# Performance work log

Hardware: AMD Instinct MI355X
Metric: run time of the kernel (lower is better)

## Reference

```python
import jax, jax.numpy as jnp
import numpy as np

STRIDE = 8.0
NUM_CLASSES = 80
IGNORE_THR = 0.5
ANCHORS = np.array([[10.,13.],[16.,30.],[33.,23.]], dtype=np.float32)
TOTAL = np.array([[10.,13.],[16.,30.],[33.,23.],[30.,61.],[62.,45.],[59.,119.],[116.,90.],[156.,198.],[373.,326.]], dtype=np.float32)
# total-anchor index -> local anchor index (anchors_mask = [0,1,2] for this head), else -1
LUT = np.array([0,1,2,-1,-1,-1,-1,-1,-1], dtype=np.int32)


def _safe_log(p):
    # matches torch BCELoss log clamping at -100 (and avoids nan grads at p==0)
    return jnp.where(p > 0, jnp.log(jnp.where(p > 0, p, 1.0)), -100.0)


def _bce(p, t):
    return -(t * _safe_log(p) + (1.0 - t) * _safe_log(1.0 - p))


def _smooth_l1(p, t):
    d = jnp.abs(p - t)
    return jnp.where(d < 1.0, 0.5 * d * d, d - 0.5)


def _iou(b1, b2):
    # center-format (cx, cy, w, h) boxes, broadcastable on leading dims
    b1x1 = b1[..., 0] - b1[..., 2] * 0.5; b1x2 = b1[..., 0] + b1[..., 2] * 0.5
    b1y1 = b1[..., 1] - b1[..., 3] * 0.5; b1y2 = b1[..., 1] + b1[..., 3] * 0.5
    b2x1 = b2[..., 0] - b2[..., 2] * 0.5; b2x2 = b2[..., 0] + b2[..., 2] * 0.5
    b2y1 = b2[..., 1] - b2[..., 3] * 0.5; b2y2 = b2[..., 1] + b2[..., 3] * 0.5
    iw = jnp.clip(jnp.minimum(b1x2, b2x2) - jnp.maximum(b1x1, b2x1), 0.0)
    ih = jnp.clip(jnp.minimum(b1y2, b2y2) - jnp.maximum(b1y1, b2y1), 0.0)
    inter = iw * ih
    a1 = (b1x2 - b1x1) * (b1y2 - b1y1)
    a2 = (b2x2 - b2x1) * (b2y2 - b2y1)
    return inter / (a1 + a2 - inter + 1e-16)


def _forward(input, targets):
    bs, _, in_h, in_w = input.shape
    A, C = ANCHORS.shape[0], NUM_CLASSES
    sa = jnp.asarray(ANCHORS) / STRIDE   # [A,2] scaled anchors
    sta = jnp.asarray(TOTAL) / STRIDE    # [9,2] scaled total anchors
    pred = input.reshape(bs, A, 5 + C, in_h, in_w).transpose(0, 1, 3, 4, 2)  # [B,A,H,W,5+C]
    x = jax.nn.sigmoid(pred[..., 0]); y = jax.nn.sigmoid(pred[..., 1])
    w = pred[..., 2]; h = pred[..., 3]
    conf = jax.nn.sigmoid(pred[..., 4])
    pred_cls = jax.nn.sigmoid(pred[..., 5:])
    gxg = jnp.arange(in_w, dtype=input.dtype)
    gyg = jnp.arange(in_h, dtype=input.dtype)
    pb_x = x + gxg[None, None, None, :]
    pb_y = y + gyg[None, None, :, None]
    pb_w = jnp.exp(w) * sa[None, :, 0, None, None]
    pb_h = jnp.exp(h) * sa[None, :, 1, None, None]
    pred_boxes = jax.lax.stop_gradient(jnp.stack([pb_x, pb_y, pb_w, pb_h], -1))  # [B,A,H,W,4] (.data in torch)

    # ---- get_target, vectorized gather/compute/scatter ----
    T = targets.shape[1]
    valid = jnp.sum(targets, -1) != 0                                     # [B,T]
    gx = targets[..., 1] * in_w; gy = targets[..., 2] * in_h
    gw = targets[..., 3] * in_w; gh = targets[..., 4] * in_h
    gi = gx.astype(jnp.int32); gj = gy.astype(jnp.int32)                  # int() truncation (gx,gy >= 0)
    # anchor matching: IoU of (0,0,gw,gh) against (0,0,aw,ah) for the 9 total anchors
    gt0 = jnp.stack([jnp.zeros_like(gw), jnp.zeros_like(gw), gw, gh], -1)  # [B,T,4]
    an0 = jnp.concatenate([jnp.zeros_like(sta), sta], -1)                  # [9,4]
    a_iou = _iou(gt0[:, :, None, :], an0[None, None, :, :])                # [B,T,9]
    best_n = jnp.argmax(a_iou, -1)                                         # [B,T]
    ai = jnp.asarray(LUT)[best_n]                                          # local anchor index or -1
    write = valid & (ai >= 0)
    ai_w = jnp.where(write, ai, A)                                         # A is OOB -> dropped scatter
    aic = jnp.clip(ai, 0, A - 1)
    # ignore mask: IoU of each gt box against all predicted boxes of its image
    gt = jnp.stack([gx, gy, gw, gh], -1)                                   # [B,T,4]
    p_iou = _iou(gt[:, :, None, None, None, :], pred_boxes[:, None])       # [B,T,A,H,W]
    ignore = jnp.any((p_iou >= IGNORE_THR) & valid[:, :, None, None, None], axis=1)  # [B,A,H,W]
    b_idx = jnp.broadcast_to(jnp.arange(bs)[:, None], (bs, T))
    z = jnp.zeros((bs, A, in_h, in_w), input.dtype)
    def scat(vals):
        return z.at[b_idx, ai_w, gj, gi].set(vals.astype(input.dtype), mode='drop')
    mask = scat(jnp.ones_like(gx))
    scales = scat(2.0 - targets[..., 3] * targets[..., 4])
    tx = scat(gx - gi.astype(input.dtype))
    ty = scat(gy - gj.astype(input.dtype))
    tw = scat(jnp.log(gw / sa[aic, 0] + 1e-16))
    th = scat(jnp.log(gh / sa[aic, 1] + 1e-16))
    cls_idx = targets[..., 0].astype(jnp.int32)
    tcls = jnp.zeros((bs, A, in_h, in_w, C), input.dtype).at[b_idx, ai_w, gj, gi, cls_idx].set(1.0, mode='drop')
    noobj = jnp.minimum(1.0 - ignore.astype(input.dtype), 1.0 - mask)
    n_obj = jnp.sum(valid).astype(input.dtype)

    loss_x = jnp.sum(scales * _bce(x * mask, tx)) / n_obj
    loss_y = jnp.sum(scales * _bce(y * mask, ty)) / n_obj
    loss_w = jnp.sum(scales * _smooth_l1(w * mask, tw)) / n_obj
    loss_h = jnp.sum(scales * _smooth_l1(h * mask, th)) / n_obj
    loss_conf = jnp.sum(_bce(conf * mask, mask)) / n_obj + 0.5 * jnp.sum(_bce(conf * noobj, jnp.zeros_like(conf))) / n_obj
    # bce(pred_cls[mask==1], tcls[mask==1]).sum() == masked full sum (bce>=0, mask binary)
    loss_cls = jnp.sum(mask[..., None] * _bce(pred_cls, tcls)) / n_obj
    loss = 2.5 * (loss_x + loss_y) + 2.5 * (loss_w + loss_h) + 1.0 * loss_conf + 1.0 * loss_cls
    return jnp.stack([loss, loss_x, loss_y, loss_w, loss_h, loss_conf, loss_cls])


def setup_inputs():
    key = jax.random.key(0)
    k1, k2 = jax.random.split(key)
    inp = jax.random.normal(k1, (16, 255, 76, 76), dtype=jnp.float32)
    tgt = jax.random.uniform(k2, (16, 50, 5), dtype=jnp.float32)  # (cls, cx, cy, w, h) in (0,1)
    return {"input": inp, "targets": tgt}


def reference(input, targets):
    return _forward(input, targets)
```

## Files before the change

kernel.cpp:

```cpp
#include <hip/hip_runtime.h>
#include <cstddef>

#define NB 16
#define NT 50
#define NA 3
#define NH 76
#define NW 76
#define NC 80
#define HWSZ (NH*NW)
#define CPB 512
#define NBLKX ((HWSZ + CPB - 1) / CPB)
#define NBLK (NBLKX * NB * NA)
#define NTARG (NB * NT)

__constant__ float d_taw[9] = {1.25f,2.0f,4.125f,3.75f,7.75f,7.375f,14.5f,19.5f,46.625f};
__constant__ float d_tah[9] = {1.625f,3.75f,2.875f,7.625f,5.625f,14.875f,11.25f,24.75f,40.75f};
__constant__ float d_saw[3] = {1.25f,2.0f,4.125f};
__constant__ float d_sah[3] = {1.625f,3.75f,2.875f};

__device__ __forceinline__ float safelog(float p) {
    return p > 0.f ? logf(p) : -100.f;
}
__device__ __forceinline__ float bce(float p, float t) {
    return -(t * safelog(p) + (1.f - t) * safelog(1.f - p));
}
__device__ __forceinline__ float sl1(float p, float t) {
    float d = fabsf(p - t);
    return d < 1.f ? 0.5f * d * d : d - 0.5f;
}
__device__ __forceinline__ float sigmoidf(float z) { return 1.f / (1.f + expf(-z)); }

struct TRec {
    bool valid, write;
    int ai, gi, gj, cls;
    float gx, gy, gw, gh;
};

__device__ __forceinline__ TRec decode(const float* __restrict__ tp) {
    TRec r;
    float t0 = tp[0], t1 = tp[1], t2 = tp[2], t3 = tp[3], t4 = tp[4];
    r.valid = (t0 + t1 + t2 + t3 + t4) != 0.f;
    r.gx = t1 * NW; r.gy = t2 * NH; r.gw = t3 * NW; r.gh = t4 * NH;
    r.gi = (int)r.gx; r.gj = (int)r.gy;
    float best = -1.f; int bn = 0;
    #pragma unroll
    for (int n = 0; n < 9; n++) {
        float inter = fminf(r.gw, d_taw[n]) * fminf(r.gh, d_tah[n]);
        float iou = inter / (r.gw * r.gh + d_taw[n] * d_tah[n] - inter + 1e-16f);
        if (iou > best) { best = iou; bn = n; }
    }
    r.ai = (bn < NA) ? bn : -1;
    r.write = r.valid && (r.ai >= 0);
    r.cls = (int)t0;
    return r;
}

__global__ __launch_bounds__(256) void k_main(const float* __restrict__ in,
                                              const float* __restrict__ tg,
                                              float* __restrict__ partials) {
    const int b = blockIdx.y / NA;
    const int a = blockIdx.y % NA;
    const int tid = threadIdx.x;
    const int base = blockIdx.x * CPB;

    __shared__ __align__(16) float st[NT][8];
    __shared__ int s_nm, s_moff[NT];
    if (tid == 0) s_nm = 0;
    __syncthreads();
    if (tid < NT) {
        TRec r = decode(tg + ((size_t)b * NT + tid) * 5);
        float x1 = r.gx - r.gw * 0.5f, y1 = r.gy - r.gh * 0.5f;
        float x2 = r.gx + r.gw * 0.5f, y2 = r.gy + r.gh * 0.5f;
        float* o = st[tid];
        o[0] = x1; o[1] = y1; o[2] = x2; o[3] = y2;
        o[4] = r.valid ? (x2 - x1) * (y2 - y1) : __builtin_inff();
        if (r.write && r.ai == a) {
            int off = r.gj * NW + r.gi - base;
            if (off >= 0 && off < CPB) {
                int slot = atomicAdd(&s_nm, 1);
                s_moff[slot] = off;
            }
        }
    }
    __syncthreads();

    const int p1 = base + tid, p2 = base + 256 + tid;
    const bool act1 = p1 < HWSZ, act2 = p2 < HWSZ;
    const int q1 = act1 ? p1 : 0, q2 = act2 ? p2 : 0;
    const float* ib = in + (size_t)(b * 255 + a * 85) * HWSZ;

    float zx1 = ib[q1], zy1 = ib[HWSZ + q1], zw1 = ib[2 * HWSZ + q1],
          zh1 = ib[3 * HWSZ + q1], zc1 = ib[4 * HWSZ + q1];
    float zx2 = ib[q2], zy2 = ib[HWSZ + q2], zw2 = ib[2 * HWSZ + q2],
          zh2 = ib[3 * HWSZ + q2], zc2 = ib[4 * HWSZ + q2];

    const int j1 = q1 / NW, i1 = q1 - j1 * NW;
    const int j2 = q2 / NW, i2 = q2 - j2 * NW;
    float x_1 = sigmoidf(zx1), y_1 = sigmoidf(zy1);
    float x_2 = sigmoidf(zx2), y_2 = sigmoidf(zy2);
    float pbx1 = x_1 + (float)i1, pby1 = y_1 + (float)j1;
    float pbx2 = x_2 + (float)i2, pby2 = y_2 + (float)j2;
    float pbw1 = expf(zw1) * d_saw[a], pbh1 = expf(zh1) * d_sah[a];
    float pbw2 = expf(zw2) * d_saw[a], pbh2 = expf(zh2) * d_sah[a];
    float px1a = pbx1 - pbw1 * 0.5f, px1b = pbx1 + pbw1 * 0.5f;
    float py1a = pby1 - pbh1 * 0.5f, py1b = pby1 + pbh1 * 0.5f;
    float px2a = pbx2 - pbw2 * 0.5f, px2b = pbx2 + pbw2 * 0.5f;
    float py2a = pby2 - pbh2 * 0.5f, py2b = pby2 + pbh2 * 0.5f;
    float pa1 = (px1b - px1a) * (py1b - py1a);
    float pa2 = (px2b - px2a) * (py2b - py2a);

    bool ig1 = false, ig2 = false;
    for (int tb = 0; tb < NT; tb += 5) {
        float4 B[5]; float A_[5];
        #pragma unroll
        for (int u = 0; u < 5; u++) {
            B[u] = *(const float4*)&st[tb + u][0];
            A_[u] = st[tb + u][4];
        }
        #pragma unroll
        for (int u = 0; u < 5; u++) {
            float iw1 = fmaxf(fminf(B[u].z, px1b) - fmaxf(B[u].x, px1a), 0.f);
            float ih1 = fmaxf(fminf(B[u].w, py1b) - fmaxf(B[u].y, py1a), 0.f);
            if (3.f * (iw1 * ih1) >= A_[u] + pa1) ig1 = true;
            float iw2 = fmaxf(fminf(B[u].z, px2b) - fmaxf(B[u].x, px2a), 0.f);
            float ih2 = fmaxf(fminf(B[u].w, py2b) - fmaxf(B[u].y, py2a), 0.f);
            if (3.f * (iw2 * ih2) >= A_[u] + pa2) ig2 = true;
        }
    }

    const int nm = s_nm;
    bool mm1 = false, mm2 = false;
    for (int e = 0; e < nm; e++) {
        int mo = s_moff[e];
        mm1 |= (mo == tid); mm2 |= (mo == tid + 256);
    }
    float lc = 0.f;
    if (act1 && !mm1 && !ig1) lc += 0.5f * (-safelog(1.f - sigmoidf(zc1)));
    if (act2 && !mm2 && !ig2) lc += 0.5f * (-safelog(1.f - sigmoidf(zc2)));

    __shared__ float red[4];
    const int wid = tid >> 6, lane = tid & 63;
    float s = lc;
    #pragma unroll
    for (int off = 32; off > 0; off >>= 1) s += __shfl_down(s, off);
    if (lane == 0) red[wid] = s;
    __syncthreads();
    if (tid == 0)
        partials[blockIdx.y * NBLKX + blockIdx.x] = red[0] + red[1] + red[2] + red[3];
}

__global__ __launch_bounds__(512) void k_final(const float* __restrict__ in,
                                               const float* __restrict__ tg,
                                               const float* __restrict__ partials,
                                               float* __restrict__ out) {
    const int tid = threadIdx.x;
    const int wid = tid >> 6, lane = tid & 63;
    __shared__ int s_nmat, s_nobj;
    __shared__ int s_mt[NTARG];
    __shared__ float s_acc[6];
    __shared__ float s_noobj;
    if (tid == 0) { s_nmat = 0; s_nobj = 0; s_noobj = 0.f; }
    if (tid < 6) s_acc[tid] = 0.f;
    __syncthreads();

    int cval = 0;
    #pragma unroll
    for (int rr = 0; rr < 2; rr++) {
        int idx = tid + rr * 512;
        if (idx < NTARG) {
            TRec tr = decode(tg + (size_t)idx * 5);
            if (tr.valid) cval++;
            if (tr.write) { int slot = atomicAdd(&s_nmat, 1); s_mt[slot] = idx; }
        }
    }
    #pragma unroll
    for (int off = 32; off > 0; off >>= 1) cval += __shfl_down(cval, off);
    if (lane == 0) atomicAdd(&s_nobj, cval);
    __syncthreads();

    const int nmat = s_nmat;
    for (int e = wid; e < nmat; e += 8) {
        const int t = s_mt[e];
        const int b = t / NT, tloc = t - b * NT;
        TRec r; r.valid = false; r.write = false;
        r.ai = -1; r.gi = -1; r.gj = -1; r.cls = 0;
        r.gx = r.gy = r.gw = r.gh = 0.f;
        float txl = 0.f, tyl = 0.f, twl = 0.f, thl = 0.f, scl = 0.f;
        if (lane < NT) {
            r = decode(tg + ((size_t)b * NT + lane) * 5);
            txl = r.gx - (float)r.gi; tyl = r.gy - (float)r.gj;
            int aic = r.ai < 0 ? 0 : r.ai;
            twl = logf(r.gw / d_saw[aic] + 1e-16f);
            thl = logf(r.gh / d_sah[aic] + 1e-16f);
            scl = 2.f - (r.gw / (float)NW) * (r.gh / (float)NH);
        }
        const int a  = __shfl(r.ai, tloc);
        const int gi = __shfl(r.gi, tloc);
        const int gj = __shfl(r.gj, tloc);
        bool match = r.write && (r.ai == a) && (r.gi == gi) && (r.gj == gj);
        unsigned long long mb = __ballot(match);
        int tlast = 63 - __clzll((long long)mb);
        if (tloc != tlast) continue;
        unsigned long long m0 = 0ull; unsigned m1 = 0u;
        unsigned long long mm = mb;
        while (mm) {
            int l = __ffsll(mm) - 1; mm &= mm - 1;
            int c = __shfl(r.cls, l);
            if (c < 64) m0 |= 1ull << c; else m1 |= 1u << (c - 64);
        }
        float tx = __shfl(txl, tlast), ty = __shfl(tyl, tlast);
        float tw = __shfl(twl, tlast), th = __shfl(thl, tlast);
        float sc = __shfl(scl, tlast);
        const size_t cb = ((size_t)b * 255 + (size_t)a * 85) * HWSZ
                        + (size_t)(gj * NW + gi);
        float z5 = (lane < 5) ? in[cb + (size_t)lane * HWSZ] : 0.f;
        float zx = __shfl(z5, 0), zy = __shfl(z5, 1), zww = __shfl(z5, 2),
              zhh = __shfl(z5, 3), zcf = __shfl(z5, 4);
        float zca = in[cb + (size_t)(5 + lane) * HWSZ];
        float zcb = (lane < 16) ? in[cb + (size_t)(69 + lane) * HWSZ] : 0.f;
        float tca = ((m0 >> lane) & 1ull) ? 1.f : 0.f;
        float lcls = bce(sigmoidf(zca), tca);
        if (lane < 16) {
            float tcb = ((m1 >> lane) & 1u) ? 1.f : 0.f;
            lcls += bce(sigmoidf(zcb), tcb);
        }
        #pragma unroll
        for (int off = 32; off > 0; off >>= 1) lcls += __shfl_down(lcls, off);
        if (lane == 0) {
            atomicAdd(&s_acc[0], sc * bce(sigmoidf(zx), tx));
            atomicAdd(&s_acc[1], sc * bce(sigmoidf(zy), ty));
            atomicAdd(&s_acc[2], sc * sl1(zww, tw));
            atomicAdd(&s_acc[3], sc * sl1(zhh, th));
            atomicAdd(&s_acc[4], -safelog(sigmoidf(zcf)));
            atomicAdd(&s_acc[5], lcls);
        }
    }

    if (wid == 0) {
        float s = 0.f;
        for (int i = lane; i < NBLK; i += 64) s += partials[i];
        #pragma unroll
        for (int off = 32; off > 0; off >>= 1) s += __shfl_down(s, off);
        if (lane == 0) s_noobj = s;
    }
    __syncthreads();
    if (tid == 0) {
        float n = (float)s_nobj;
        float lx = s_acc[0] / n, ly = s_acc[1] / n;
        float lw = s_acc[2] / n, lh = s_acc[3] / n;
        float lcf = (s_acc[4] + s_noobj) / n, lcl = s_acc[5] / n;
        out[0] = 2.5f * (lx + ly) + 2.5f * (lw + lh) + lcf + lcl;
        out[1] = lx; out[2] = ly; out[3] = lw; out[4] = lh; out[5] = lcf; out[6] = lcl;
    }
}

extern "C" void kernel_launch(void* const* d_in, const int* in_sizes, int n_in,
                              void* d_out, int out_size, void* d_ws, size_t ws_size,
                              hipStream_t stream) {
    const float* input   = (const float*)d_in[0];
    const float* targets = (const float*)d_in[1];
    float* out = (float*)d_out;
    float* ws  = (float*)d_ws;

    dim3 grid(NBLKX, NB * NA);
    k_main<<<grid, 256, 0, stream>>>(input, targets, ws);
    k_final<<<1, 512, 0, stream>>>(input, targets, ws, out);
}
```

Baseline: 149.2 us.

## Move positive-target loss into extra block of main kernel, shrink final reduce

New measurement: 146.0 us. 1.02x faster.

```diff
diff --git a/kernel.cpp b/kernel.cpp
--- a/kernel.cpp
+++ b/kernel.cpp
@@ -8,10 +8,12 @@
 #define NW 76
 #define NC 80
 #define HWSZ (NH*NW)
-#define CPB 512
+#define CPB 1024
 #define NBLKX ((HWSZ + CPB - 1) / CPB)
 #define NBLK (NBLKX * NB * NA)
 #define NTARG (NB * NT)
+#define WS_ACC  NBLK
+#define WS_NOBJ (NBLK + 6)
 
 __constant__ float d_taw[9] = {1.25f,2.0f,4.125f,3.75f,7.75f,7.375f,14.5f,19.5f,46.625f};
 __constant__ float d_tah[9] = {1.625f,3.75f,2.875f,7.625f,5.625f,14.875f,11.25f,24.75f,40.75f};
@@ -57,14 +59,105 @@
 
 __global__ __launch_bounds__(256) void k_main(const float* __restrict__ in,
                                               const float* __restrict__ tg,
-                                              float* __restrict__ partials) {
+                                              float* __restrict__ ws) {
+    const int tid = threadIdx.x;
+    const int wid = tid >> 6, lane = tid & 63;
+
+    __shared__ __align__(16) float st[NT][8];
+    __shared__ int s_nm, s_moff[NT];
+    __shared__ float red[4];
+    __shared__ int s_nmat, s_nobj;
+    __shared__ int s_mt[NTARG];
+    __shared__ float s_acc[6];
+
+    if (blockIdx.y == NB * NA) {
+        if (blockIdx.x != 0) return;
+        if (tid == 0) { s_nmat = 0; s_nobj = 0; }
+        if (tid < 6) s_acc[tid] = 0.f;
+        __syncthreads();
+
+        int cval = 0;
+        #pragma unroll
+        for (int rr = 0; rr < 4; rr++) {
+            int idx = tid + rr * 256;
+            if (idx < NTARG) {
+                TRec tr = decode(tg + (size_t)idx * 5);
+                if (tr.valid) cval++;
+                if (tr.write) { int slot = atomicAdd(&s_nmat, 1); s_mt[slot] = idx; }
+            }
+        }
+        #pragma unroll
+        for (int off = 32; off > 0; off >>= 1) cval += __shfl_down(cval, off);
+        if (lane == 0) atomicAdd(&s_nobj, cval);
+        __syncthreads();
+
+        const int nmat = s_nmat;
+        for (int e = wid; e < nmat; e += 4) {
+            const int t = s_mt[e];
+            const int b = t / NT, tloc = t - b * NT;
+            TRec r; r.valid = false; r.write = false;
+            r.ai = -1; r.gi = -1; r.gj = -1; r.cls = 0;
+            r.gx = r.gy = r.gw = r.gh = 0.f;
+            float txl = 0.f, tyl = 0.f, twl = 0.f, thl = 0.f, scl = 0.f;
+            if (lane < NT) {
+                r = decode(tg + ((size_t)b * NT + lane) * 5);
+                txl = r.gx - (float)r.gi; tyl = r.gy - (float)r.gj;
+                int aic = r.ai < 0 ? 0 : r.ai;
+                twl = logf(r.gw / d_saw[aic] + 1e-16f);
+                thl = logf(r.gh / d_sah[aic] + 1e-16f);
+                scl = 2.f - (r.gw / (float)NW) * (r.gh / (float)NH);
+            }
+            const int a  = __shfl(r.ai, tloc);
+            const int gi = __shfl(r.gi, tloc);
+            const int gj = __shfl(r.gj, tloc);
+            bool match = r.write && (r.ai == a) && (r.gi == gi) && (r.gj == gj);
+            unsigned long long mb = __ballot(match);
+            int tlast = 63 - __clzll((long long)mb);
+            if (tloc != tlast) continue;
+            unsigned long long m0 = 0ull; unsigned m1 = 0u;
+            unsigned long long mm = mb;
+            while (mm) {
+                int l = __ffsll(mm) - 1; mm &= mm - 1;
+                int c = __shfl(r.cls, l);
+                if (c < 64) m0 |= 1ull << c; else m1 |= 1u << (c - 64);
+            }
+            float tx = __shfl(txl, tlast), ty = __shfl(tyl, tlast);
+            float tw = __shfl(twl, tlast), th = __shfl(thl, tlast);
+            float sc = __shfl(scl, tlast);
+            const size_t cb = ((size_t)b * 255 + (size_t)a * 85) * HWSZ
+                            + (size_t)(gj * NW + gi);
+            float z5 = (lane < 5) ? in[cb + (size_t)lane * HWSZ] : 0.f;
+            float zx = __shfl(z5, 0), zy = __shfl(z5, 1), zww = __shfl(z5, 2),
+                  zhh = __shfl(z5, 3), zcf = __shfl(z5, 4);
+            float zca = in[cb + (size_t)(5 + lane) * HWSZ];
+            float zcb = (lane < 16) ? in[cb + (size_t)(69 + lane) * HWSZ] : 0.f;
+            float tca = ((m0 >> lane) & 1ull) ? 1.f : 0.f;
+            float lcls = bce(sigmoidf(zca), tca);
+            if (lane < 16) {
+                float tcb = ((m1 >> lane) & 1u) ? 1.f : 0.f;
+                lcls += bce(sigmoidf(zcb), tcb);
+            }
+            #pragma unroll
+            for (int off = 32; off > 0; off >>= 1) lcls += __shfl_down(lcls, off);
+            if (lane == 0) {
+                atomicAdd(&s_acc[0], sc * bce(sigmoidf(zx), tx));
+                atomicAdd(&s_acc[1], sc * bce(sigmoidf(zy), ty));
+                atomicAdd(&s_acc[2], sc * sl1(zww, tw));
+                atomicAdd(&s_acc[3], sc * sl1(zhh, th));
+                atomicAdd(&s_acc[4], -safelog(sigmoidf(zcf)));
+                atomicAdd(&s_acc[5], lcls);
+            }
+        }
+        __syncthreads();
+        if (tid < 6) ws[WS_ACC + tid] = s_acc[tid];
+        if (tid == 6) ws[WS_NOBJ] = (float)s_nobj;
+        return;
+    }
+
     const int b = blockIdx.y / NA;
     const int a = blockIdx.y % NA;
-    const int tid = threadIdx.x;
     const int base = blockIdx.x * CPB;
 
-    __shared__ __align__(16) float st[NT][8];
-    __shared__ int s_nm, s_moff[NT];
     if (tid == 0) s_nm = 0;
     __syncthreads();
     if (tid < NT) {
@@ -84,32 +177,27 @@
     }
     __syncthreads();
 
-    const int p1 = base + tid, p2 = base + 256 + tid;
-    const bool act1 = p1 < HWSZ, act2 = p2 < HWSZ;
-    const int q1 = act1 ? p1 : 0, q2 = act2 ? p2 : 0;
     const float* ib = in + (size_t)(b * 255 + a * 85) * HWSZ;
-
-    float zx1 = ib[q1], zy1 = ib[HWSZ + q1], zw1 = ib[2 * HWSZ + q1],
-          zh1 = ib[3 * HWSZ + q1], zc1 = ib[4 * HWSZ + q1];
-    float zx2 = ib[q2], zy2 = ib[HWSZ + q2], zw2 = ib[2 * HWSZ + q2],
-          zh2 = ib[3 * HWSZ + q2], zc2 = ib[4 * HWSZ + q2];
-
-    const int j1 = q1 / NW, i1 = q1 - j1 * NW;
-    const int j2 = q2 / NW, i2 = q2 - j2 * NW;
-    float x_1 = sigmoidf(zx1), y_1 = sigmoidf(zy1);
-    float x_2 = sigmoidf(zx2), y_2 = sigmoidf(zy2);
-    float pbx1 = x_1 + (float)i1, pby1 = y_1 + (float)j1;
-    float pbx2 = x_2 + (float)i2, pby2 = y_2 + (float)j2;
-    float pbw1 = expf(zw1) * d_saw[a], pbh1 = expf(zh1) * d_sah[a];
-    float pbw2 = expf(zw2) * d_saw[a], pbh2 = expf(zh2) * d_sah[a];
-    float px1a = pbx1 - pbw1 * 0.5f, px1b = pbx1 + pbw1 * 0.5f;
-    float py1a = pby1 - pbh1 * 0.5f, py1b = pby1 + pbh1 * 0.5f;
-    float px2a = pbx2 - pbw2 * 0.5f, px2b = pbx2 + pbw2 * 0.5f;
-    float py2a = pby2 - pbh2 * 0.5f, py2b = pby2 + pbh2 * 0.5f;
-    float pa1 = (px1b - px1a) * (py1b - py1a);
-    float pa2 = (px2b - px2a) * (py2b - py2a);
-
-    bool ig1 = false, ig2 = false;
+    bool act[4]; int q[4];
+    float zc[4], pxa[4], pxb[4], pya[4], pyb[4], pa[4];
+    #pragma unroll
+    for (int c = 0; c < 4; c++) {
+        int p = base + c * 256 + tid;
+        act[c] = p < HWSZ;
+        q[c] = act[c] ? p : 0;
+        float zx = ib[q[c]], zy = ib[HWSZ + q[c]], zw = ib[2 * HWSZ + q[c]],
+              zh = ib[3 * HWSZ + q[c]];
+        zc[c] = ib[4 * HWSZ + q[c]];
+        int j = q[c] / NW, i = q[c] - j * NW;
+        float x = sigmoidf(zx), y = sigmoidf(zy);
+        float pbx = x + (float)i, pby = y + (float)j;
+        float pbw = expf(zw) * d_saw[a], pbh = expf(zh) * d_sah[a];
+        pxa[c] = pbx - pbw * 0.5f; pxb[c] = pbx + pbw * 0.5f;
+        pya[c] = pby - pbh * 0.5f; pyb[c] = pby + pbh * 0.5f;
+        pa[c] = (pxb[c] - pxa[c]) * (pyb[c] - pya[c]);
+    }
+
+    bool ig[4] = {false, false, false, false};
     for (int tb = 0; tb < NT; tb += 5) {
         float4 B[5]; float A_[5];
         #pragma unroll
@@ -119,136 +207,48 @@
         }
         #pragma unroll
         for (int u = 0; u < 5; u++) {
-            float iw1 = fmaxf(fminf(B[u].z, px1b) - fmaxf(B[u].x, px1a), 0.f);
-            float ih1 = fmaxf(fminf(B[u].w, py1b) - fmaxf(B[u].y, py1a), 0.f);
-            if (3.f * (iw1 * ih1) >= A_[u] + pa1) ig1 = true;
-            float iw2 = fmaxf(fminf(B[u].z, px2b) - fmaxf(B[u].x, px2a), 0.f);
-            float ih2 = fmaxf(fminf(B[u].w, py2b) - fmaxf(B[u].y, py2a), 0.f);
-            if (3.f * (iw2 * ih2) >= A_[u] + pa2) ig2 = true;
+            #pragma unroll
+            for (int c = 0; c < 4; c++) {
+                float iw = fmaxf(fminf(B[u].z, pxb[c]) - fmaxf(B[u].x, pxa[c]), 0.f);
+                float ih = fmaxf(fminf(B[u].w, pyb[c]) - fmaxf(B[u].y, pya[c]), 0.f);
+                if (3.f * (iw * ih) >= A_[u] + pa[c]) ig[c] = true;
+            }
         }
     }
 
     const int nm = s_nm;
-    bool mm1 = false, mm2 = false;
+    bool mm[4] = {false, false, false, false};
     for (int e = 0; e < nm; e++) {
         int mo = s_moff[e];
-        mm1 |= (mo == tid); mm2 |= (mo == tid + 256);
+        #pragma unroll
+        for (int c = 0; c < 4; c++) mm[c] |= (mo == c * 256 + tid);
     }
     float lc = 0.f;
-    if (act1 && !mm1 && !ig1) lc += 0.5f * (-safelog(1.f - sigmoidf(zc1)));
-    if (act2 && !mm2 && !ig2) lc += 0.5f * (-safelog(1.f - sigmoidf(zc2)));
-
-    __shared__ float red[4];
-    const int wid = tid >> 6, lane = tid & 63;
+    #pragma unroll
+    for (int c = 0; c < 4; c++)
+        if (act[c] && !mm[c] && !ig[c]) lc += 0.5f * (-safelog(1.f - sigmoidf(zc[c])));
+
     float s = lc;
     #pragma unroll
     for (int off = 32; off > 0; off >>= 1) s += __shfl_down(s, off);
     if (lane == 0) red[wid] = s;
     __syncthreads();
     if (tid == 0)
-        partials[blockIdx.y * NBLKX + blockIdx.x] = red[0] + red[1] + red[2] + red[3];
-}
-
-__global__ __launch_bounds__(512) void k_final(const float* __restrict__ in,
-                                               const float* __restrict__ tg,
-                                               const float* __restrict__ partials,
-                                               float* __restrict__ out) {
-    const int tid = threadIdx.x;
-    const int wid = tid >> 6, lane = tid & 63;
-    __shared__ int s_nmat, s_nobj;
-    __shared__ int s_mt[NTARG];
-    __shared__ float s_acc[6];
-    __shared__ float s_noobj;
-    if (tid == 0) { s_nmat = 0; s_nobj = 0; s_noobj = 0.f; }
-    if (tid < 6) s_acc[tid] = 0.f;
-    __syncthreads();
-
-    int cval = 0;
-    #pragma unroll
-    for (int rr = 0; rr < 2; rr++) {
-        int idx = tid + rr * 512;
-        if (idx < NTARG) {
-            TRec tr = decode(tg + (size_t)idx * 5);
-            if (tr.valid) cval++;
-            if (tr.write) { int slot = atomicAdd(&s_nmat, 1); s_mt[slot] = idx; }
-        }
-    }
-    #pragma unroll
-    for (int off = 32; off > 0; off >>= 1) cval += __shfl_down(cval, off);
-    if (lane == 0) atomicAdd(&s_nobj, cval);
-    __syncthreads();
-
-    const int nmat = s_nmat;
-    for (int e = wid; e < nmat; e += 8) {
-        const int t = s_mt[e];
-        const int b = t / NT, tloc = t - b * NT;
-        TRec r; r.valid = false; r.write = false;
-        r.ai = -1; r.gi = -1; r.gj = -1; r.cls = 0;
-        r.gx = r.gy = r.gw = r.gh = 0.f;
-        float txl = 0.f, tyl = 0.f, twl = 0.f, thl = 0.f, scl = 0.f;
-        if (lane < NT) {
-            r = decode(tg + ((size_t)b * NT + lane) * 5);
-            txl = r.gx - (float)r.gi; tyl = r.gy - (float)r.gj;
-            int aic = r.ai < 0 ? 0 : r.ai;
-            twl = logf(r.gw / d_saw[aic] + 1e-16f);
-            thl = logf(r.gh / d_sah[aic] + 1e-16f);
-            scl = 2.f - (r.gw / (float)NW) * (r.gh / (float)NH);
-        }
-        const int a  = __shfl(r.ai, tloc);
-        const int gi = __shfl(r.gi, tloc);
-        const int gj = __shfl(r.gj, tloc);
-        bool match = r.write && (r.ai == a) && (r.gi == gi) && (r.gj == gj);
-        unsigned long long mb = __ballot(match);
-        int tlast = 63 - __clzll((long long)mb);
-        if (tloc != tlast) continue;
-        unsigned long long m0 = 0ull; unsigned m1 = 0u;
-        unsigned long long mm = mb;
-        while (mm) {
-            int l = __ffsll(mm) - 1; mm &= mm - 1;
-            int c = __shfl(r.cls, l);
-            if (c < 64) m0 |= 1ull << c; else m1 |= 1u << (c - 64);
-        }
-        float tx = __shfl(txl, tlast), ty = __shfl(tyl, tlast);
-        float tw = __shfl(twl, tlast), th = __shfl(thl, tlast);
-        float sc = __shfl(scl, tlast);
-        const size_t cb = ((size_t)b * 255 + (size_t)a * 85) * HWSZ
-                        + (size_t)(gj * NW + gi);
-        float z5 = (lane < 5) ? in[cb + (size_t)lane * HWSZ] : 0.f;
-        float zx = __shfl(z5, 0), zy = __shfl(z5, 1), zww = __shfl(z5, 2),
-              zhh = __shfl(z5, 3), zcf = __shfl(z5, 4);
-        float zca = in[cb + (size_t)(5 + lane) * HWSZ];
-        float zcb = (lane < 16) ? in[cb + (size_t)(69 + lane) * HWSZ] : 0.f;
-        float tca = ((m0 >> lane) & 1ull) ? 1.f : 0.f;
-        float lcls = bce(sigmoidf(zca), tca);
-        if (lane < 16) {
-            float tcb = ((m1 >> lane) & 1u) ? 1.f : 0.f;
-            lcls += bce(sigmoidf(zcb), tcb);
-        }
-        #pragma unroll
-        for (int off = 32; off > 0; off >>= 1) lcls += __shfl_down(lcls, off);
-        if (lane == 0) {
-            atomicAdd(&s_acc[0], sc * bce(sigmoidf(zx), tx));
-            atomicAdd(&s_acc[1], sc * bce(sigmoidf(zy), ty));
-            atomicAdd(&s_acc[2], sc * sl1(zww, tw));
-            atomicAdd(&s_acc[3], sc * sl1(zhh, th));
-            atomicAdd(&s_acc[4], -safelog(sigmoidf(zcf)));
-            atomicAdd(&s_acc[5], lcls);
-        }
-    }
-
-    if (wid == 0) {
-        float s = 0.f;
-        for (int i = lane; i < NBLK; i += 64) s += partials[i];
-        #pragma unroll
-        for (int off = 32; off > 0; off >>= 1) s += __shfl_down(s, off);
-        if (lane == 0) s_noobj = s;
-    }
-    __syncthreads();
-    if (tid == 0) {
-        float n = (float)s_nobj;
-        float lx = s_acc[0] / n, ly = s_acc[1] / n;
-        float lw = s_acc[2] / n, lh = s_acc[3] / n;
-        float lcf = (s_acc[4] + s_noobj) / n, lcl = s_acc[5] / n;
+        ws[blockIdx.y * NBLKX + blockIdx.x] = red[0] + red[1] + red[2] + red[3];
+}
+
+__global__ __launch_bounds__(64) void k_final(const float* __restrict__ ws,
+                                              float* __restrict__ out) {
+    const int lane = threadIdx.x;
+    float s = 0.f;
+    for (int i = lane; i < NBLK; i += 64) s += ws[i];
+    #pragma unroll
+    for (int off = 32; off > 0; off >>= 1) s += __shfl_down(s, off);
+    if (lane == 0) {
+        float n = ws[WS_NOBJ];
+        float lx = ws[WS_ACC + 0] / n, ly = ws[WS_ACC + 1] / n;
+        float lw = ws[WS_ACC + 2] / n, lh = ws[WS_ACC + 3] / n;
+        float lcf = (ws[WS_ACC + 4] + s) / n, lcl = ws[WS_ACC + 5] / n;
         out[0] = 2.5f * (lx + ly) + 2.5f * (lw + lh) + lcf + lcl;
         out[1] = lx; out[2] = ly; out[3] = lw; out[4] = lh; out[5] = lcf; out[6] = lcl;
     }
@@ -262,7 +262,7 @@
     float* out = (float*)d_out;
     float* ws  = (float*)d_ws;
 
-    dim3 grid(NBLKX, NB * NA);
+    dim3 grid(NBLKX, NB * NA + 1);
     k_main<<<grid, 256, 0, stream>>>(input, targets, ws);
-    k_final<<<1, 512, 0, stream>>>(input, targets, ws, out);
-}
+    k_final<<<1, 64, 0, stream>>>(ws, out);
+}
```
